# Kernel tuning notes

Hardware: AMD Instinct MI355X
Metric: run time of the kernel (lower is better)

The kernel has to match this reference:

```python
import jax, jax.numpy as jnp
import numpy as np

U, I, D, E, B = 100000, 50000, 128, 3200000, 4096
KEEP_PROB = 0.8

def setup_inputs() -> dict:
    key = jax.random.key(0)
    ks = jax.random.split(key, 9)
    return {
        "user_emb": 0.01 * jax.random.normal(ks[0], (U, D), dtype=jnp.float32),
        "item_emb": 0.01 * jax.random.normal(ks[1], (I, D), dtype=jnp.float32),
        "vals": jax.random.uniform(ks[2], (E,), dtype=jnp.float32),
        "keep_mask": jax.random.uniform(ks[3], (E,), dtype=jnp.float32),
        "rows": jax.random.randint(ks[4], (E,), 0, U, dtype=jnp.int32),
        "cols": jax.random.randint(ks[5], (E,), 0, I, dtype=jnp.int32),
        "user": jax.random.randint(ks[6], (B,), 0, U, dtype=jnp.int32),
        "pos_item": jax.random.randint(ks[7], (B,), 0, I, dtype=jnp.int32),
        "neg_item": jax.random.randint(ks[8], (B,), 0, I, dtype=jnp.int32),
    }

def reference(user_emb, item_emb, vals, keep_mask, rows, cols, user, pos_item, neg_item):
    # Edge dropout: keep edge iff uniform < keep_prob, rescale by 1/keep_prob.
    # (Equivalent to torch's index filtering, expressed as zeroed values.)
    dvals = jnp.where(keep_mask < KEEP_PROB, vals / KEEP_PROB, 0.0)
    u0, i0 = user_emb, item_emb
    # i_1 = spmm(A^T, u_0): scatter edge messages by item (col) index.  [I, D]
    i1 = jax.ops.segment_sum(dvals[:, None] * u0[rows], cols, num_segments=item_emb.shape[0])
    # u_1 = spmm(A, i_0): scatter edge messages by user (row) index.    [U, D]
    u1 = jax.ops.segment_sum(dvals[:, None] * i0[cols], rows, num_segments=user_emb.shape[0])
    # Layer combination (mean of layer-0 and layer-1), gathered per batch.
    u = (u0[user] + u1[user]) * 0.5        # [B, D]
    i = (i0[pos_item] + i1[pos_item]) * 0.5
    j = (i0[neg_item] + i1[neg_item]) * 0.5
    pos_score = jnp.sum(u * i, axis=1, keepdims=True)  # [B, 1]
    neg_score = jnp.sum(u * j, axis=1, keepdims=True)  # [B, 1]
    return (pos_score, neg_score)
```

## Files before the change

### kernel.cpp

```cpp
#include <hip/hip_runtime.h>

#define DIM 128
#define KEEP_PROB 0.8f
#define UCAP 96
#define ICAP 160

__global__ void slot_kernel(const int* __restrict__ user, const int* __restrict__ pos,
                            const int* __restrict__ neg, int* __restrict__ u_slot,
                            int* __restrict__ i_slot, unsigned* __restrict__ u_mask,
                            unsigned* __restrict__ i_mask, int B) {
    int t = blockIdx.x * blockDim.x + threadIdx.x;
    if (t < B) {
        int u = user[t];
        u_slot[u] = t;
        atomicOr(&u_mask[u >> 5], 1u << (u & 31));
    } else if (t < 2 * B) {
        int it = pos[t - B];
        i_slot[it] = t - B;
        atomicOr(&i_mask[it >> 5], 1u << (it & 31));
    } else if (t < 3 * B) {
        int it = neg[t - 2 * B];
        i_slot[it] = (t - 2 * B) + B;
        atomicOr(&i_mask[it >> 5], 1u << (it & 31));
    }
}

__global__ void fill_bucket_kernel(const float* __restrict__ vals, const float* __restrict__ keep,
                                   const int* __restrict__ rows, const int* __restrict__ cols,
                                   const int* __restrict__ u_slot, const int* __restrict__ i_slot,
                                   const unsigned* __restrict__ u_mask,
                                   const unsigned* __restrict__ i_mask,
                                   int* __restrict__ cursor, int2* __restrict__ entries,
                                   int E, int B) {
    int t = blockIdx.x * blockDim.x + threadIdx.x;
    int base = t * 8;
    if (base >= E) return;
    long long ib = (long long)B * UCAP;
    if (base + 7 < E) {
        float4 ka = *(const float4*)(keep + base), kb = *(const float4*)(keep + base + 4);
        float4 va = *(const float4*)(vals + base), vb = *(const float4*)(vals + base + 4);
        int4 ra = *(const int4*)(rows + base), rb = *(const int4*)(rows + base + 4);
        int4 ca = *(const int4*)(cols + base), cb = *(const int4*)(cols + base + 4);
        float kk[8] = {ka.x, ka.y, ka.z, ka.w, kb.x, kb.y, kb.z, kb.w};
        float vv[8] = {va.x, va.y, va.z, va.w, vb.x, vb.y, vb.z, vb.w};
        int rr[8] = {ra.x, ra.y, ra.z, ra.w, rb.x, rb.y, rb.z, rb.w};
        int cc[8] = {ca.x, ca.y, ca.z, ca.w, cb.x, cb.y, cb.z, cb.w};
#pragma unroll
        for (int j = 0; j < 8; j++) {
            if (kk[j] < KEEP_PROB) {
                int r = rr[j], c = cc[j];
                float dv = vv[j] * 1.25f;
                if ((u_mask[r >> 5] >> (r & 31)) & 1u) {
                    int us = u_slot[r];
                    int p = atomicAdd(&cursor[us], 1);
                    if (p < UCAP) entries[(long long)us * UCAP + p] = make_int2(c, __float_as_int(dv));
                }
                if ((i_mask[c >> 5] >> (c & 31)) & 1u) {
                    int is = i_slot[c];
                    int p = atomicAdd(&cursor[B + is], 1);
                    if (p < ICAP) entries[ib + (long long)is * ICAP + p] = make_int2(r, __float_as_int(dv));
                }
            }
        }
    } else {
        for (int e = base; e < E; e++) {
            if (keep[e] < KEEP_PROB) {
                int r = rows[e], c = cols[e];
                float dv = vals[e] * 1.25f;
                if ((u_mask[r >> 5] >> (r & 31)) & 1u) {
                    int us = u_slot[r];
                    int p = atomicAdd(&cursor[us], 1);
                    if (p < UCAP) entries[(long long)us * UCAP + p] = make_int2(c, __float_as_int(dv));
                }
                if ((i_mask[c >> 5] >> (c & 31)) & 1u) {
                    int is = i_slot[c];
                    int p = atomicAdd(&cursor[B + is], 1);
                    if (p < ICAP) entries[ib + (long long)is * ICAP + p] = make_int2(r, __float_as_int(dv));
                }
            }
        }
    }
}

__global__ void count_kernel(const float* __restrict__ keep, const int* __restrict__ rows,
                             const int* __restrict__ cols, const int* __restrict__ u_slot,
                             const int* __restrict__ i_slot, int* __restrict__ cnt,
                             int E, int B) {
    int t = blockIdx.x * blockDim.x + threadIdx.x;
    int base = t * 4;
    if (base >= E) return;
    for (int e = base; e < base + 4 && e < E; e++) {
        if (keep[e] < KEEP_PROB) {
            int us = u_slot[rows[e]];
            if (us >= 0) atomicAdd(&cnt[us], 1);
            int is = i_slot[cols[e]];
            if (is >= 0) atomicAdd(&cnt[B + is], 1);
        }
    }
}

__global__ void scan_kernel(const int* __restrict__ cnt, int* __restrict__ offs,
                            int* __restrict__ cursor, int n) {
    __shared__ int wave_tot[16];
    __shared__ int carry_s;
    int tid = threadIdx.x, lane = tid & 63, wv = tid >> 6;
    if (tid == 0) carry_s = 0;
    __syncthreads();
    for (int base = 0; base < n; base += 1024) {
        int v = (base + tid < n) ? cnt[base + tid] : 0;
        int x = v;
#pragma unroll
        for (int off = 1; off < 64; off <<= 1) {
            int y = __shfl_up(x, off);
            if (lane >= off) x += y;
        }
        if (lane == 63) wave_tot[wv] = x;
        __syncthreads();
        if (wv == 0 && lane < 16) {
            int tot = wave_tot[lane];
            int s = tot;
#pragma unroll
            for (int off = 1; off < 16; off <<= 1) {
                int y = __shfl_up(s, off);
                if (lane >= off) s += y;
            }
            wave_tot[lane] = s - tot;
        }
        __syncthreads();
        int excl = (x - v) + wave_tot[wv] + carry_s;
        if (base + tid < n) { offs[base + tid] = excl; cursor[base + tid] = excl; }
        __syncthreads();
        if (tid == 1023) carry_s += wave_tot[15] + x;
        __syncthreads();
    }
}

__global__ void fill_csr_kernel(const float* __restrict__ vals, const float* __restrict__ keep,
                                const int* __restrict__ rows, const int* __restrict__ cols,
                                const int* __restrict__ u_slot, const int* __restrict__ i_slot,
                                int* __restrict__ cursor, int2* __restrict__ entries,
                                long long cap, int E, int B) {
    int t = blockIdx.x * blockDim.x + threadIdx.x;
    int base = t * 4;
    if (base >= E) return;
    for (int e = base; e < base + 4 && e < E; e++) {
        if (keep[e] < KEEP_PROB) {
            float dv = vals[e] * 1.25f;
            int us = u_slot[rows[e]];
            if (us >= 0) {
                int p = atomicAdd(&cursor[us], 1);
                if (p < cap) entries[p] = make_int2(cols[e], __float_as_int(dv));
            }
            int is = i_slot[cols[e]];
            if (is >= 0) {
                int p = atomicAdd(&cursor[B + is], 1);
                if (p < cap) entries[p] = make_int2(rows[e], __float_as_int(dv));
            }
        }
    }
}

__global__ void gather_kernel(const int2* __restrict__ entries, const int* __restrict__ offs,
                              const int* __restrict__ cntp, const float* __restrict__ u0,
                              const float* __restrict__ i0, float* __restrict__ u1c,
                              float* __restrict__ i1c, int B, int mode, long long cap) {
    __shared__ float part[2][DIM];
    int pair = threadIdx.x >> 7;
    int half = (threadIdx.x >> 6) & 1;
    int lane = threadIdx.x & 63;
    int dest = blockIdx.x * 2 + pair;

    const float* table;
    float* dst;
    if (dest < B) { table = i0; dst = u1c + (size_t)dest * DIM; }
    else          { table = u0; dst = i1c + (size_t)(dest - B) * DIM; }

    int n = cntp[dest];
    long long base;
    if (mode == 1) {
        if (dest < B) { base = (long long)dest * UCAP; if (n > UCAP) n = UCAP; }
        else { base = (long long)B * UCAP + (long long)(dest - B) * ICAP; if (n > ICAP) n = ICAP; }
    } else {
        base = offs[dest];
        if (base + n > cap) { long long rem = cap - base; n = rem < 0 ? 0 : (int)rem; }
    }

    int m = (n - half + 1) >> 1;
    int o = lane * 2;
    float ax = 0.f, ay = 0.f;
    for (int k0 = 0; k0 < m; k0 += 64) {
        int my = k0 + lane;
        int2 e = make_int2(0, 0);
        if (my < m) e = entries[base + half + 2 * (long long)my];
        int mm = m - k0;
        if (mm > 64) mm = 64;
        int j = 0;
        for (; j + 8 <= mm; j += 8) {
            int s0 = __shfl(e.x, j + 0), s1 = __shfl(e.x, j + 1);
            int s2 = __shfl(e.x, j + 2), s3 = __shfl(e.x, j + 3);
            int s4 = __shfl(e.x, j + 4), s5 = __shfl(e.x, j + 5);
            int s6 = __shfl(e.x, j + 6), s7 = __shfl(e.x, j + 7);
            float d0 = __int_as_float(__shfl(e.y, j + 0));
            float d1 = __int_as_float(__shfl(e.y, j + 1));
            float d2 = __int_as_float(__shfl(e.y, j + 2));
            float d3 = __int_as_float(__shfl(e.y, j + 3));
            float d4 = __int_as_float(__shfl(e.y, j + 4));
            float d5 = __int_as_float(__shfl(e.y, j + 5));
            float d6 = __int_as_float(__shfl(e.y, j + 6));
            float d7 = __int_as_float(__shfl(e.y, j + 7));
            float2 r0 = *(const float2*)(table + (size_t)s0 * DIM + o);
            float2 r1 = *(const float2*)(table + (size_t)s1 * DIM + o);
            float2 r2 = *(const float2*)(table + (size_t)s2 * DIM + o);
            float2 r3 = *(const float2*)(table + (size_t)s3 * DIM + o);
            float2 r4 = *(const float2*)(table + (size_t)s4 * DIM + o);
            float2 r5 = *(const float2*)(table + (size_t)s5 * DIM + o);
            float2 r6 = *(const float2*)(table + (size_t)s6 * DIM + o);
            float2 r7 = *(const float2*)(table + (size_t)s7 * DIM + o);
            ax += d0 * r0.x; ay += d0 * r0.y;
            ax += d1 * r1.x; ay += d1 * r1.y;
            ax += d2 * r2.x; ay += d2 * r2.y;
            ax += d3 * r3.x; ay += d3 * r3.y;
            ax += d4 * r4.x; ay += d4 * r4.y;
            ax += d5 * r5.x; ay += d5 * r5.y;
            ax += d6 * r6.x; ay += d6 * r6.y;
            ax += d7 * r7.x; ay += d7 * r7.y;
        }
        for (; j < mm; j++) {
            int s = __shfl(e.x, j);
            float dv = __int_as_float(__shfl(e.y, j));
            float2 r = *(const float2*)(table + (size_t)s * DIM + o);
            ax += dv * r.x; ay += dv * r.y;
        }
    }
    if (half == 1) { part[pair][o] = ax; part[pair][o + 1] = ay; }
    __syncthreads();
    if (half == 0) {
        ax += part[pair][o];
        ay += part[pair][o + 1];
        *(float2*)(dst + o) = make_float2(ax, ay);
    }
}

__global__ void score_kernel(const float* __restrict__ u0, const float* __restrict__ i0,
                             const float* __restrict__ u1c, const float* __restrict__ i1c,
                             const int* __restrict__ user, const int* __restrict__ pos,
                             const int* __restrict__ neg, const int* __restrict__ u_slot,
                             const int* __restrict__ i_slot, float* __restrict__ out, int B) {
    int wave = (blockIdx.x * blockDim.x + threadIdx.x) >> 6;
    int lane = threadIdx.x & 63;
    if (wave >= B) return;

    int ub = user[wave], pb = pos[wave], nb = neg[wave];
    int usl = u_slot[ub], psl = i_slot[pb], nsl = i_slot[nb];
    int o = lane * 2;

    float2 a0 = *(const float2*)(u0  + (size_t)ub  * DIM + o);
    float2 a1 = *(const float2*)(u1c + (size_t)usl * DIM + o);
    float2 p0 = *(const float2*)(i0  + (size_t)pb  * DIM + o);
    float2 p1 = *(const float2*)(i1c + (size_t)psl * DIM + o);
    float2 n0 = *(const float2*)(i0  + (size_t)nb  * DIM + o);
    float2 n1 = *(const float2*)(i1c + (size_t)nsl * DIM + o);

    float ux = (a0.x + a1.x) * 0.5f, uy = (a0.y + a1.y) * 0.5f;
    float px = (p0.x + p1.x) * 0.5f, py = (p0.y + p1.y) * 0.5f;
    float nx = (n0.x + n1.x) * 0.5f, ny = (n0.y + n1.y) * 0.5f;

    float ps = ux * px + uy * py;
    float ns = ux * nx + uy * ny;
    for (int off = 32; off > 0; off >>= 1) {
        ps += __shfl_down(ps, off);
        ns += __shfl_down(ns, off);
    }
    if (lane == 0) {
        out[wave]     = ps;
        out[B + wave] = ns;
    }
}

extern "C" void kernel_launch(void* const* d_in, const int* in_sizes, int n_in,
                              void* d_out, int out_size, void* d_ws, size_t ws_size,
                              hipStream_t stream) {
    const float* user_emb = (const float*)d_in[0];
    const float* item_emb = (const float*)d_in[1];
    const float* vals     = (const float*)d_in[2];
    const float* keep     = (const float*)d_in[3];
    const int*   rows     = (const int*)d_in[4];
    const int*   cols     = (const int*)d_in[5];
    const int*   user     = (const int*)d_in[6];
    const int*   pos      = (const int*)d_in[7];
    const int*   neg      = (const int*)d_in[8];
    float* out = (float*)d_out;

    int U = in_sizes[0] / DIM;
    int I = in_sizes[1] / DIM;
    int E = in_sizes[2];
    int B = in_sizes[6];

    int umw = ((U + 31) / 32 + 3) & ~3;
    int imw = ((I + 31) / 32 + 3) & ~3;

    char* p = (char*)d_ws;
    int* u_slot = (int*)p;              p += (size_t)U * 4;
    int* i_slot = (int*)p;              p += (size_t)I * 4;
    unsigned* u_mask = (unsigned*)p;    p += (size_t)umw * 4;
    unsigned* i_mask = (unsigned*)p;    p += (size_t)imw * 4;
    int* cnt    = (int*)p;              p += (size_t)3 * B * 4;
    int* offs   = (int*)p;              p += (size_t)3 * B * 4;
    int* cursor = (int*)p;              p += (size_t)3 * B * 4;
    float* u1c  = (float*)p;            p += (size_t)B * DIM * 4;
    float* i1c  = (float*)p;            p += (size_t)2 * B * DIM * 4;
    int2* entries = (int2*)p;
    size_t used = (size_t)(p - (char*)d_ws);
    long long avail = (long long)ws_size - (long long)used;

    long long bucket_entries = (long long)B * UCAP + (long long)2 * B * ICAP;
    int mode = (avail >= bucket_entries * (long long)sizeof(int2)) ? 1 : 0;

    hipMemsetAsync(u_slot, 0xFF, (size_t)(U + I) * 4, stream);
    hipMemsetAsync(u_mask, 0x00, (size_t)(umw + imw + 9 * B) * 4, stream);

    slot_kernel<<<(3 * B + 255) / 256, 256, 0, stream>>>(user, pos, neg, u_slot, i_slot,
                                                         u_mask, i_mask, B);

    long long cap;
    if (mode == 1) {
        cap = bucket_entries;
        int fb = ((E + 7) / 8 + 255) / 256;
        fill_bucket_kernel<<<fb, 256, 0, stream>>>(vals, keep, rows, cols, u_slot, i_slot,
                                                   u_mask, i_mask, cursor, entries, E, B);
        gather_kernel<<<(3 * B) / 2, 256, 0, stream>>>(entries, offs, cursor, user_emb,
                                                       item_emb, u1c, i1c, B, 1, cap);
    } else {
        cap = avail / (long long)sizeof(int2);
        if (cap < 0) cap = 0;
        int cb = ((E + 3) / 4 + 255) / 256;
        count_kernel<<<cb, 256, 0, stream>>>(keep, rows, cols, u_slot, i_slot, cnt, E, B);
        scan_kernel<<<1, 1024, 0, stream>>>(cnt, offs, cursor, 3 * B);
        fill_csr_kernel<<<cb, 256, 0, stream>>>(vals, keep, rows, cols, u_slot, i_slot,
                                                cursor, entries, cap, E, B);
        gather_kernel<<<(3 * B) / 2, 256, 0, stream>>>(entries, offs, cnt, user_emb,
                                                       item_emb, u1c, i1c, B, 0, cap);
    }

    score_kernel<<<(B * 64 + 255) / 256, 256, 0, stream>>>(user_emb, item_emb, u1c, i1c,
                                                           user, pos, neg, u_slot, i_slot,
                                                           out, B);
}
```

Measured before the change: 220.2 us.

## Cache batch masks in LDS, split each gather destination across four waves

The fill kernel now copies the user and item membership bitmasks into shared memory once per block and runs its per-edge lookups there instead of in global memory. The gather kernel assigns one destination per 256-thread block, splitting its edge list across four waves with a 4-way unroll, instead of two waves per destination with an 8-way unroll. The 0xFF memset of the slot tables is skipped in bucket mode, because slots are only read where a mask bit is set. The trade-off is that every fill block reloads roughly 18 KB of masks, and the gather launches twice as many blocks, each with less unrolled memory-level parallelism per wave.

```diff
diff --git a/kernel.cpp b/kernel.cpp
--- a/kernel.cpp
+++ b/kernel.cpp
@@ -4,6 +4,7 @@
 #define KEEP_PROB 0.8f
 #define UCAP 96
 #define ICAP 160
+#define SMASK_WORDS 5120
 
 __global__ void slot_kernel(const int* __restrict__ user, const int* __restrict__ pos,
                             const int* __restrict__ neg, int* __restrict__ u_slot,
@@ -25,13 +26,23 @@
     }
 }
 
+template <bool LDS>
 __global__ void fill_bucket_kernel(const float* __restrict__ vals, const float* __restrict__ keep,
                                    const int* __restrict__ rows, const int* __restrict__ cols,
                                    const int* __restrict__ u_slot, const int* __restrict__ i_slot,
-                                   const unsigned* __restrict__ u_mask,
-                                   const unsigned* __restrict__ i_mask,
+                                   const unsigned* __restrict__ masks, int umw, int mw_total,
                                    int* __restrict__ cursor, int2* __restrict__ entries,
                                    int E, int B) {
+    __shared__ unsigned sm[LDS ? SMASK_WORDS : 1];
+    const unsigned *um, *im;
+    if constexpr (LDS) {
+        for (int i = threadIdx.x; i < mw_total; i += blockDim.x) sm[i] = masks[i];
+        __syncthreads();
+        um = sm; im = sm + umw;
+    } else {
+        um = masks; im = masks + umw;
+    }
+
     int t = blockIdx.x * blockDim.x + threadIdx.x;
     int base = t * 8;
     if (base >= E) return;
@@ -50,12 +61,12 @@
             if (kk[j] < KEEP_PROB) {
                 int r = rr[j], c = cc[j];
                 float dv = vv[j] * 1.25f;
-                if ((u_mask[r >> 5] >> (r & 31)) & 1u) {
+                if ((um[r >> 5] >> (r & 31)) & 1u) {
                     int us = u_slot[r];
                     int p = atomicAdd(&cursor[us], 1);
                     if (p < UCAP) entries[(long long)us * UCAP + p] = make_int2(c, __float_as_int(dv));
                 }
-                if ((i_mask[c >> 5] >> (c & 31)) & 1u) {
+                if ((im[c >> 5] >> (c & 31)) & 1u) {
                     int is = i_slot[c];
                     int p = atomicAdd(&cursor[B + is], 1);
                     if (p < ICAP) entries[ib + (long long)is * ICAP + p] = make_int2(r, __float_as_int(dv));
@@ -67,12 +78,12 @@
             if (keep[e] < KEEP_PROB) {
                 int r = rows[e], c = cols[e];
                 float dv = vals[e] * 1.25f;
-                if ((u_mask[r >> 5] >> (r & 31)) & 1u) {
+                if ((um[r >> 5] >> (r & 31)) & 1u) {
                     int us = u_slot[r];
                     int p = atomicAdd(&cursor[us], 1);
                     if (p < UCAP) entries[(long long)us * UCAP + p] = make_int2(c, __float_as_int(dv));
                 }
-                if ((i_mask[c >> 5] >> (c & 31)) & 1u) {
+                if ((im[c >> 5] >> (c & 31)) & 1u) {
                     int is = i_slot[c];
                     int p = atomicAdd(&cursor[B + is], 1);
                     if (p < ICAP) entries[ib + (long long)is * ICAP + p] = make_int2(r, __float_as_int(dv));
@@ -164,11 +175,10 @@
                               const int* __restrict__ cntp, const float* __restrict__ u0,
                               const float* __restrict__ i0, float* __restrict__ u1c,
                               float* __restrict__ i1c, int B, int mode, long long cap) {
-    __shared__ float part[2][DIM];
-    int pair = threadIdx.x >> 7;
-    int half = (threadIdx.x >> 6) & 1;
+    __shared__ float part[3][DIM];
+    int wv = threadIdx.x >> 6;
     int lane = threadIdx.x & 63;
-    int dest = blockIdx.x * 2 + pair;
+    int dest = blockIdx.x;
 
     const float* table;
     float* dst;
@@ -182,48 +192,35 @@
         else { base = (long long)B * UCAP + (long long)(dest - B) * ICAP; if (n > ICAP) n = ICAP; }
     } else {
         base = offs[dest];
-        if (base + n > cap) { long long rem = cap - base; n = rem < 0 ? 0 : (int)rem; }
-    }
-
-    int m = (n - half + 1) >> 1;
+        if (base + (long long)n > cap) { long long rem = cap - base; n = rem < 0 ? 0 : (int)rem; }
+    }
+
+    int m = (n - wv + 3) >> 2;
+    if (m < 0) m = 0;
     int o = lane * 2;
     float ax = 0.f, ay = 0.f;
     for (int k0 = 0; k0 < m; k0 += 64) {
         int my = k0 + lane;
         int2 e = make_int2(0, 0);
-        if (my < m) e = entries[base + half + 2 * (long long)my];
+        if (my < m) e = entries[base + wv + 4 * (long long)my];
         int mm = m - k0;
         if (mm > 64) mm = 64;
         int j = 0;
-        for (; j + 8 <= mm; j += 8) {
+        for (; j + 4 <= mm; j += 4) {
             int s0 = __shfl(e.x, j + 0), s1 = __shfl(e.x, j + 1);
             int s2 = __shfl(e.x, j + 2), s3 = __shfl(e.x, j + 3);
-            int s4 = __shfl(e.x, j + 4), s5 = __shfl(e.x, j + 5);
-            int s6 = __shfl(e.x, j + 6), s7 = __shfl(e.x, j + 7);
             float d0 = __int_as_float(__shfl(e.y, j + 0));
             float d1 = __int_as_float(__shfl(e.y, j + 1));
             float d2 = __int_as_float(__shfl(e.y, j + 2));
             float d3 = __int_as_float(__shfl(e.y, j + 3));
-            float d4 = __int_as_float(__shfl(e.y, j + 4));
-            float d5 = __int_as_float(__shfl(e.y, j + 5));
-            float d6 = __int_as_float(__shfl(e.y, j + 6));
-            float d7 = __int_as_float(__shfl(e.y, j + 7));
             float2 r0 = *(const float2*)(table + (size_t)s0 * DIM + o);
             float2 r1 = *(const float2*)(table + (size_t)s1 * DIM + o);
             float2 r2 = *(const float2*)(table + (size_t)s2 * DIM + o);
             float2 r3 = *(const float2*)(table + (size_t)s3 * DIM + o);
-            float2 r4 = *(const float2*)(table + (size_t)s4 * DIM + o);
-            float2 r5 = *(const float2*)(table + (size_t)s5 * DIM + o);
-            float2 r6 = *(const float2*)(table + (size_t)s6 * DIM + o);
-            float2 r7 = *(const float2*)(table + (size_t)s7 * DIM + o);
             ax += d0 * r0.x; ay += d0 * r0.y;
             ax += d1 * r1.x; ay += d1 * r1.y;
             ax += d2 * r2.x; ay += d2 * r2.y;
             ax += d3 * r3.x; ay += d3 * r3.y;
-            ax += d4 * r4.x; ay += d4 * r4.y;
-            ax += d5 * r5.x; ay += d5 * r5.y;
-            ax += d6 * r6.x; ay += d6 * r6.y;
-            ax += d7 * r7.x; ay += d7 * r7.y;
         }
         for (; j < mm; j++) {
             int s = __shfl(e.x, j);
@@ -232,11 +229,11 @@
             ax += dv * r.x; ay += dv * r.y;
         }
     }
-    if (half == 1) { part[pair][o] = ax; part[pair][o + 1] = ay; }
+    if (wv > 0) { part[wv - 1][o] = ax; part[wv - 1][o + 1] = ay; }
     __syncthreads();
-    if (half == 0) {
-        ax += part[pair][o];
-        ay += part[pair][o + 1];
+    if (wv == 0) {
+        ax += part[0][o] + part[1][o] + part[2][o];
+        ay += part[0][o + 1] + part[1][o + 1] + part[2][o + 1];
         *(float2*)(dst + o) = make_float2(ax, ay);
     }
 }
@@ -316,8 +313,8 @@
     long long bucket_entries = (long long)B * UCAP + (long long)2 * B * ICAP;
     int mode = (avail >= bucket_entries * (long long)sizeof(int2)) ? 1 : 0;
 
-    hipMemsetAsync(u_slot, 0xFF, (size_t)(U + I) * 4, stream);
     hipMemsetAsync(u_mask, 0x00, (size_t)(umw + imw + 9 * B) * 4, stream);
+    if (mode == 0) hipMemsetAsync(u_slot, 0xFF, (size_t)(U + I) * 4, stream);
 
     slot_kernel<<<(3 * B + 255) / 256, 256, 0, stream>>>(user, pos, neg, u_slot, i_slot,
                                                          u_mask, i_mask, B);
@@ -326,10 +323,17 @@
     if (mode == 1) {
         cap = bucket_entries;
         int fb = ((E + 7) / 8 + 255) / 256;
-        fill_bucket_kernel<<<fb, 256, 0, stream>>>(vals, keep, rows, cols, u_slot, i_slot,
-                                                   u_mask, i_mask, cursor, entries, E, B);
-        gather_kernel<<<(3 * B) / 2, 256, 0, stream>>>(entries, offs, cursor, user_emb,
-                                                       item_emb, u1c, i1c, B, 1, cap);
+        if (umw + imw <= SMASK_WORDS) {
+            fill_bucket_kernel<true><<<fb, 256, 0, stream>>>(vals, keep, rows, cols, u_slot,
+                                                             i_slot, u_mask, umw, umw + imw,
+                                                             cursor, entries, E, B);
+        } else {
+            fill_bucket_kernel<false><<<fb, 256, 0, stream>>>(vals, keep, rows, cols, u_slot,
+                                                              i_slot, u_mask, umw, umw + imw,
+                                                              cursor, entries, E, B);
+        }
+        gather_kernel<<<3 * B, 256, 0, stream>>>(entries, offs, cursor, user_emb, item_emb,
+                                                 u1c, i1c, B, 1, cap);
     } else {
         cap = avail / (long long)sizeof(int2);
         if (cap < 0) cap = 0;
@@ -338,8 +342,8 @@
         scan_kernel<<<1, 1024, 0, stream>>>(cnt, offs, cursor, 3 * B);
         fill_csr_kernel<<<cb, 256, 0, stream>>>(vals, keep, rows, cols, u_slot, i_slot,
                                                 cursor, entries, cap, E, B);
-        gather_kernel<<<(3 * B) / 2, 256, 0, stream>>>(entries, offs, cnt, user_emb,
-                                                       item_emb, u1c, i1c, B, 0, cap);
+        gather_kernel<<<3 * B, 256, 0, stream>>>(entries, offs, cnt, user_emb, item_emb,
+                                                 u1c, i1c, B, 0, cap);
     }
 
     score_kernel<<<(B * 64 + 255) / 256, 256, 0, stream>>>(user_emb, item_emb, u1c, i1c,
```

After: 219.6 us. Within noise of the previous version (-0.2%).
